# Performance work log

Measured on AMD Instinct MI355X. Metric: run time of the kernel, lower is better.

Reference implementation:

```python
import jax, jax.numpy as jnp
import numpy as np

B, N, C = 4, 1024, 1024
H, TD, MULT = 16, 256, 4
HD = C // H
MAX_LEN = 1024
EPS = 1e-5


def _layer_norm(x, g, b):
    m = jnp.mean(x, axis=-1, keepdims=True)
    v = jnp.mean((x - m) ** 2, axis=-1, keepdims=True)
    return (x - m) / jnp.sqrt(v + EPS) * g + b


def _skew(x):
    # x: [B,H,N,M] -> pad left on last dim, reshape, drop first row -> [B,H,N,M]
    b, h, n, m = x.shape
    x = jnp.pad(x, ((0, 0), (0, 0), (0, 0), (1, 0)))
    x = x.reshape(b, h, m + 1, n)
    return x[:, :, 1:, :]


def setup_inputs() -> dict:
    key = jax.random.key(0)
    ks = jax.random.split(key, 16)
    s = 0.02
    return {
        "x": jax.random.normal(ks[0], (B, N, C), jnp.float32),
        "t": jax.random.normal(ks[1], (B, TD), jnp.float32),
        "ln1_g": jnp.ones((C,), jnp.float32),
        "ln1_b": jnp.zeros((C,), jnp.float32),
        "qkv_w": jax.random.normal(ks[2], (C, 3 * C), jnp.float32) * s,
        "qkv_b": jnp.zeros((3 * C,), jnp.float32),
        "time_w": jax.random.normal(ks[3], (TD, 3 * C), jnp.float32) * s,
        "time_b": jnp.zeros((3 * C,), jnp.float32),
        "out_w": jax.random.normal(ks[4], (C, C), jnp.float32) * s,
        "out_b": jnp.zeros((C,), jnp.float32),
        "Er": jax.random.normal(ks[5], (MAX_LEN, HD), jnp.float32) * s,
        "ln2_g": jnp.ones((C,), jnp.float32),
        "ln2_b": jnp.zeros((C,), jnp.float32),
        "ff1_w": jax.random.normal(ks[6], (C, MULT * C), jnp.float32) * s,
        "ff1_b": jnp.zeros((MULT * C,), jnp.float32),
        "ff2_w": jax.random.normal(ks[7], (MULT * C, C), jnp.float32) * s,
        "ff2_b": jnp.zeros((C,), jnp.float32),
    }


def reference(x, t, ln1_g, ln1_b, qkv_w, qkv_b, time_w, time_b, out_w, out_b,
              Er, ln2_g, ln2_b, ff1_w, ff1_b, ff2_w, ff2_b):
    # ---- attention branch ----
    xn = _layer_norm(x, ln1_g, ln1_b)
    qkv = (xn @ qkv_w + qkv_b).reshape(B, N, 3, H, HD).transpose(2, 0, 3, 1, 4)
    q, k, v = qkv[0], qkv[1], qkv[2]  # [B,H,N,HD]
    tqkv = (t @ time_w + time_b).reshape(B, 1, 3, H, HD).transpose(2, 0, 3, 1, 4)
    q = q + tqkv[0]
    k = k + tqkv[1]
    v = v + tqkv[2]
    Er_n = Er[MAX_LEN - N:]  # [N,HD]
    rel = jnp.einsum('bhnd,md->bhnm', q, Er_n)
    rel = _skew(rel)
    scale = HD ** -0.5
    attn = jnp.einsum('bhnd,bhmd->bhnm', q, k) * scale + rel
    attn = jax.nn.softmax(attn, axis=-1)
    out = jnp.einsum('bhnm,bhmd->bhnd', attn, v)
    out = out.transpose(0, 2, 1, 3).reshape(B, N, C)
    x = x + (out @ out_w + out_b)
    # ---- FFN branch ----
    h = _layer_norm(x, ln2_g, ln2_b)
    h = jax.nn.gelu(h @ ff1_w + ff1_b, approximate=False)
    x = x + (h @ ff2_w + ff2_b)
    return x
```

## Files before the change

### kernel.cpp

```cpp
#include <hip/hip_runtime.h>
#include <hip/hip_bf16.h>

typedef __attribute__((ext_vector_type(8))) short short8;
typedef __attribute__((ext_vector_type(4))) float f32x4;
typedef __attribute__((ext_vector_type(16))) float f32x16;

#define DEV __device__ __forceinline__

DEV float bf2f(ushort u){ union { float f; unsigned int i; } x; x.i = ((unsigned int)u)<<16; return x.f; }
DEV ushort f2bf(float f){ union { float fl; unsigned int i; } x; x.fl = f; unsigned int r = x.i + 0x7fffu + ((x.i>>16)&1u); return (ushort)(r>>16); }

DEV void gl2lds16(const ushort* g, ushort* l){
  __builtin_amdgcn_global_load_lds((const __attribute__((address_space(1))) void*)g,
                                   (__attribute__((address_space(3))) void*)l, 16, 0, 0);
}
DEV f32x16 mfma32(short8 a, short8 b, f32x16 c){
  return __builtin_amdgcn_mfma_f32_32x32x16_bf16(a, b, c, 0, 0, 0);
}
DEV uint cvtpk(float lo, float hi){
  uint r; asm("v_cvt_pk_bf16_f32 %0, %1, %2" : "=v"(r) : "v"(lo), "v"(hi));
  return r;
}

__global__ void cvt_f2b(const float* __restrict__ in, ushort* __restrict__ out, int n){
  int i = blockIdx.x*blockDim.x + threadIdx.x;
  int stride = gridDim.x*blockDim.x;
  for (; i < n; i += stride) out[i] = f2bf(in[i]);
}

__global__ __launch_bounds__(256) void wt_cvt(const float* __restrict__ in, ushort* __restrict__ out,
                                              int K, int N, int ldk){
  const int n0 = blockIdx.x*64, k0 = blockIdx.y*64;
  __shared__ float T[64][65];
  const int tid = threadIdx.x;
  const int r = tid>>4, c = (tid&15)*4;
  #pragma unroll
  for (int p=0;p<4;p++){
    float4 v = *(const float4*)&in[(size_t)(k0 + p*16 + r)*N + n0 + c];
    T[p*16+r][c+0]=v.x; T[p*16+r][c+1]=v.y; T[p*16+r][c+2]=v.z; T[p*16+r][c+3]=v.w;
  }
  __syncthreads();
  #pragma unroll
  for (int p=0;p<4;p++){
    int n = p*16 + r;
    ushort u0 = f2bf(T[c+0][n]), u1 = f2bf(T[c+1][n]), u2 = f2bf(T[c+2][n]), u3 = f2bf(T[c+3][n]);
    ushort4 u = make_ushort4(u0,u1,u2,u3);
    *(ushort4*)&out[(size_t)(n0+n)*ldk + k0 + c] = u;
  }
}

__global__ __launch_bounds__(256) void vt_k(const ushort* __restrict__ qkv, ushort* __restrict__ vt){
  const int bh = blockIdx.y; const int b = bh>>4, h = bh&15;
  const int n0 = blockIdx.x*64;
  __shared__ ushort T[64][66];
  const int tid = threadIdx.x;
  const int r = tid>>3, c8 = (tid&7)*8;
  #pragma unroll
  for (int p=0;p<2;p++){
    int row = p*32 + r;
    short8 v = *(const short8*)&qkv[(size_t)(b*1024 + n0 + row)*3200 + 2048 + h*64 + c8];
    #pragma unroll
    for (int i=0;i<8;i++) T[row][c8+i] = ((ushort*)&v)[i];
  }
  __syncthreads();
  #pragma unroll
  for (int p=0;p<2;p++){
    int d = p*32 + r;
    union { ushort u[8]; short8 v; } o;
    #pragma unroll
    for (int i=0;i<8;i++) o.u[i] = T[c8+i][d];
    *(short8*)&vt[(size_t)(bh*64 + d)*1152 + n0 + c8] = o.v;
  }
}

__global__ __launch_bounds__(256) void ln_rows(const float* __restrict__ in,
                                               const float* __restrict__ g,
                                               const float* __restrict__ bta,
                                               ushort* __restrict__ out, int ldo){
  int row = blockIdx.x; int tid = threadIdx.x;
  const float* x = in + (size_t)row*1024;
  float v[4]; float s = 0.f;
  #pragma unroll
  for (int i=0;i<4;i++){ v[i] = x[tid + 256*i]; s += v[i]; }
  __shared__ float rbuf[256];
  rbuf[tid] = s; __syncthreads();
  for (int off=128; off>0; off>>=1){ if (tid<off) rbuf[tid]+=rbuf[tid+off]; __syncthreads(); }
  float mean = rbuf[0] * (1.f/1024.f);
  __syncthreads();
  float s2 = 0.f;
  #pragma unroll
  for (int i=0;i<4;i++){ float d=v[i]-mean; s2 += d*d; }
  rbuf[tid] = s2; __syncthreads();
  for (int off=128; off>0; off>>=1){ if (tid<off) rbuf[tid]+=rbuf[tid+off]; __syncthreads(); }
  float var = rbuf[0] * (1.f/1024.f);
  float rstd = rsqrtf(var + 1e-5f);
  #pragma unroll
  for (int i=0;i<4;i++){ int c = tid+256*i; out[(size_t)row*ldo+c] = f2bf((v[i]-mean)*rstd*g[c]+bta[c]); }
}

__global__ __launch_bounds__(256) void tq_gemm2(const float* __restrict__ t, const float* __restrict__ tw,
                                                const float* __restrict__ tb, float* __restrict__ tq){
  const int tid = threadIdx.x;
  const int j = blockIdx.x*64 + (tid & 63);
  const int sl = tid >> 6;
  float acc[4] = {0.f,0.f,0.f,0.f};
  for (int k = sl*64; k < sl*64+64; ++k){
    float wv = tw[(size_t)k*3072 + j];
    #pragma unroll
    for (int b=0;b<4;b++) acc[b] = fmaf(t[b*256+k], wv, acc[b]);
  }
  __shared__ float red[4][4][64];
  #pragma unroll
  for (int b=0;b<4;b++) red[sl][b][tid&63] = acc[b];
  __syncthreads();
  if (sl == 0){
    #pragma unroll
    for (int b=0;b<4;b++)
      tq[b*3072 + j] = red[0][b][tid&63] + red[1][b][tid&63] + red[2][b][tid&63] + red[3][b][tid&63] + tb[j];
  }
}

template<int EPI, int TN>
__global__ __launch_bounds__(256) void gemm4(
    const ushort* __restrict__ A, const ushort* __restrict__ Bt,
    const float* __restrict__ bias, const float* __restrict__ extra,
    ushort* __restrict__ outb, float* __restrict__ outf,
    int K, int lda, int ldb, int ldo, int lde, int nbx)
{
  constexpr int NJ = TN/32;
  __shared__ __align__(16) ushort Al[2][128*32];
  __shared__ __align__(16) ushort Bl[2][TN*32];
  const int nwg = gridDim.x, cpx = nwg >> 3;
  const int bid = blockIdx.x;
  const int swz = (bid & 7)*cpx + (bid >> 3);
  const int m0 = (swz / nbx)*128, n0 = (swz % nbx)*TN;
  const int tid = threadIdx.x, lane = tid & 63, wid = tid >> 6;
  const int wm = (wid&1)*64, wn = (wid>>1)*(TN/2);
  const int l15 = lane&15, l4 = lane>>4;
  f32x4 acc[4][NJ];
  #pragma unroll
  for (int i=0;i<4;i++)
    #pragma unroll
    for (int jx=0;jx<NJ;jx++){ acc[i][jx][0]=0.f; acc[i][jx][1]=0.f; acc[i][jx][2]=0.f; acc[i][jx][3]=0.f; }
  const ushort* a0p = A + (size_t)(m0 + (tid>>2))*lda + (tid&3)*8;
  const ushort* a1p = A + (size_t)(m0 + 64 + (tid>>2))*lda + (tid&3)*8;
  const ushort* b0p = Bt + (size_t)(n0 + (tid>>2))*ldb + (tid&3)*8;
  const ushort* b1p = nullptr;
  if constexpr (TN==128) b1p = Bt + (size_t)(n0 + 64 + (tid>>2))*ldb + (tid&3)*8;
  const int lsl = tid*8, lsh = (tid+256)*8;

  gl2lds16(a0p, &Al[0][lsl]);
  gl2lds16(a1p, &Al[0][lsh]);
  gl2lds16(b0p, &Bl[0][lsl]);
  if constexpr (TN==128) gl2lds16(b1p, &Bl[0][lsh]);
  __syncthreads();

  const int nk = K >> 5;
  for (int it=0; it<nk; ++it){
    const int cur = it & 1;
    ushort* Ac = Al[cur];  ushort* Bc = Bl[cur];
    if (it+1 < nk){
      const int k1 = (it+1) << 5;
      gl2lds16(a0p + k1, &Al[cur^1][lsl]);
      gl2lds16(a1p + k1, &Al[cur^1][lsh]);
      gl2lds16(b0p + k1, &Bl[cur^1][lsl]);
      if constexpr (TN==128) gl2lds16(b1p + k1, &Bl[cur^1][lsh]);
    }
    short8 af[4], bfr[NJ];
    #pragma unroll
    for (int mi=0;mi<4;mi++) af[mi]  = *(const short8*)&Ac[(wm + mi*16 + l15)*32 + l4*8];
    #pragma unroll
    for (int nj=0;nj<NJ;nj++) bfr[nj] = *(const short8*)&Bc[(wn + nj*16 + l15)*32 + l4*8];
    #pragma unroll
    for (int mi=0;mi<4;mi++)
      #pragma unroll
      for (int nj=0;nj<NJ;nj++)
        acc[mi][nj] = __builtin_amdgcn_mfma_f32_16x16x32_bf16(af[mi], bfr[nj], acc[mi][nj], 0,0,0);
    __syncthreads();
  }
  #pragma unroll
  for (int mi=0;mi<4;mi++)
    #pragma unroll
    for (int nj=0;nj<NJ;nj++)
      #pragma unroll
      for (int j=0;j<4;j++){
        int row = m0 + wm + mi*16 + l4*4 + j;
        int col = n0 + wn + nj*16 + l15;
        float v = acc[mi][nj][j] + bias[col];
        if constexpr (EPI==0){ v += extra[(size_t)(row>>10)*lde + col]; outb[(size_t)row*ldo+col] = f2bf(v); }
        else if constexpr (EPI==1){ v += extra[(size_t)row*lde + col]; outf[(size_t)row*ldo+col] = v; }
        else { v = 0.5f*v*(1.f+erff(v*0.70710678118f)); outb[(size_t)row*ldo+col] = f2bf(v); }
      }
}


__global__ __launch_bounds__(256) void relskew(
    const ushort* __restrict__ qkv, const ushort* __restrict__ Er,
    ushort* __restrict__ srel)
{
  const int bid0 = blockIdx.x;
  const int bid = ((bid0 & 7) << 9) | (bid0 >> 3);
  const int rt = bid & 63, h = (bid>>6)&15, b = bid>>10;
  const int bh = b*16 + h;
  const int r0 = rt*16;
  const int tid = threadIdx.x, w = tid>>6, lane = tid&63;
  const int l15 = lane&15, l4 = lane>>4;
  __shared__ __align__(16) ushort T[17*1032];
  ushort* srb = srel + (size_t)bh*1024*1040;

  if (tid < 17){
    int tgt = r0 - 1 + tid;
    int c = tgt + 1;
    if (tgt >= 0 && c <= 1023) T[tid*1032 + c] = 0;
  }
  const ushort* Qp = qkv + (size_t)b*1024*3200 + h*64;
  short8 qa0 = *(const short8*)(Qp + (size_t)(r0+l15)*3200 + l4*8);
  short8 qa1 = *(const short8*)(Qp + (size_t)(r0+l15)*3200 + 32 + l4*8);
  for (int t=0;t<16;++t){
    const int et = w*16 + t;
    short8 e0 = *(const short8*)(Er + (size_t)(et*16+l15)*64 + l4*8);
    short8 e1 = *(const short8*)(Er + (size_t)(et*16+l15)*64 + 32 + l4*8);
    f32x4 a0 = {0.f,0.f,0.f,0.f};
    a0 = __builtin_amdgcn_mfma_f32_16x16x32_bf16(qa0, e0, a0, 0,0,0);
    a0 = __builtin_amdgcn_mfma_f32_16x16x32_bf16(qa1, e1, a0, 0,0,0);
    const int e = et*16 + l15;
    #pragma unroll
    for (int j=0;j<4;j++){
      int lr = 4*l4 + j;
      int r = r0 + lr;
      ushort v = f2bf(a0[j] * 1.4426950408f);
      bool below = (e >= 1023 - r);
      int ldsrow = below ? (lr + 1) : lr;
      int c = below ? (e + r - 1023) : (e + r + 1);
      T[ldsrow*1032 + c] = v;
    }
  }
  __syncthreads();
  const int c4 = tid*4;
  for (int i=0;i<17;++i){
    int tgt = r0 - 1 + i;
    if (tgt < 0) continue;
    int lo = (i==0) ? (r0+1) : 0;
    int hh = (i==16) ? min(r0+16,1023) : 1023;
    if (c4 >= lo && c4+3 <= hh){
      uint2 vv = *(const uint2*)&T[i*1032 + c4];
      *(uint2*)(srb + (size_t)tgt*1040 + c4) = vv;
    } else if (c4 <= hh && c4+3 >= lo){
      #pragma unroll
      for (int k2=0;k2<4;k2++){
        int c = c4 + k2;
        if (c >= lo && c <= hh) srb[(size_t)tgt*1040 + c] = T[i*1032 + c];
      }
    }
  }
}

__global__ __launch_bounds__(256) void attn6(
    const ushort* __restrict__ qkv, const ushort* __restrict__ srel,
    const ushort* __restrict__ Vt, ushort* __restrict__ out)
{
  const int bid0 = blockIdx.x;
  const int swz = (bid0 & 7)*64 + (bid0 >> 3);
  const int bh = swz >> 3, b = bh >> 4, h = bh & 15;
  const int rblk = (swz & 7)*128;
  const int tid = threadIdx.x, w = tid >> 6, lane = tid & 63;
  const int l31 = lane & 31, hi = lane >> 5;
  const int r = rblk + w*32 + l31;
  const ushort* Qp = qkv + (size_t)b*1024*3200 + h*64;
  const ushort* Kp = Qp + 1024;
  const ushort* Vp = Vt + (size_t)bh*64*1152;
  const ushort* Bp = srel + (size_t)bh*1024*1040 + (size_t)r*1040 + hi*4;

  short8 qf0 = *(const short8*)(Qp + (size_t)r*3200 +      hi*8);
  short8 qf1 = *(const short8*)(Qp + (size_t)r*3200 + 16 + hi*8);
  short8 qf2 = *(const short8*)(Qp + (size_t)r*3200 + 32 + hi*8);
  short8 qf3 = *(const short8*)(Qp + (size_t)r*3200 + 48 + hi*8);

  f32x16 O0 = {}, O1 = {};
  float m = -3e38f, lsum = 0.f;

  short8 kA0 = *(const short8*)(Kp + (size_t)l31*3200 +      hi*8);
  short8 kA1 = *(const short8*)(Kp + (size_t)l31*3200 + 16 + hi*8);
  short8 kA2 = *(const short8*)(Kp + (size_t)l31*3200 + 32 + hi*8);
  short8 kA3 = *(const short8*)(Kp + (size_t)l31*3200 + 48 + hi*8);
  short8 kB0, kB1, kB2, kB3;

  auto step = [&](short8& ka0, short8& ka1, short8& ka2, short8& ka3,
                  short8& kn0, short8& kn1, short8& kn2, short8& kn3, int t){
    const int c0 = t*32;
    if (t < 31){
      const ushort* kp = Kp + (size_t)(c0 + 32 + l31)*3200 + hi*8;
      kn0 = *(const short8*)(kp);
      kn1 = *(const short8*)(kp + 16);
      kn2 = *(const short8*)(kp + 32);
      kn3 = *(const short8*)(kp + 48);
    }
    ushort4 bs[4];
    #pragma unroll
    for (int rq=0;rq<4;rq++) bs[rq] = *(const ushort4*)(Bp + c0 + rq*8);
    short8 v00 = *(const short8*)(Vp + (size_t)l31*1152      + c0 +      hi*8);
    short8 v01 = *(const short8*)(Vp + (size_t)l31*1152      + c0 + 16 + hi*8);
    short8 v10 = *(const short8*)(Vp + (size_t)(32+l31)*1152 + c0 +      hi*8);
    short8 v11 = *(const short8*)(Vp + (size_t)(32+l31)*1152 + c0 + 16 + hi*8);
    f32x16 S = {};
    S = mfma32(ka0, qf0, S);
    S = mfma32(ka1, qf1, S);
    S = mfma32(ka2, qf2, S);
    S = mfma32(ka3, qf3, S);
    float p[16];
    float tmax = -3e38f;
    #pragma unroll
    for (int rq=0;rq<4;rq++)
      #pragma unroll
      for (int j=0;j<4;j++){
        float v = fmaf(S[rq*4+j], 0.18033688f, bf2f(((const ushort*)&bs[rq])[j]));
        p[rq*4+j] = v;
        tmax = fmaxf(tmax, v);
      }
    tmax = fmaxf(tmax, __shfl_xor(tmax, 32, 64));
    if (!__all(tmax <= m + 8.f)){
      float mn = fmaxf(m, tmax);
      float scl = __builtin_amdgcn_exp2f(m - mn);
      m = mn; lsum *= scl;
      #pragma unroll
      for (int i=0;i<16;i++){ O0[i]*=scl; O1[i]*=scl; }
    }
    float tsum = 0.f;
    #pragma unroll
    for (int reg=0;reg<16;reg++){ p[reg] = __builtin_amdgcn_exp2f(p[reg]-m); tsum += p[reg]; }
    lsum += tsum;
    uint W00=cvtpk(p[0],p[1]),   W01=cvtpk(p[2],p[3]);
    uint W10=cvtpk(p[4],p[5]),   W11=cvtpk(p[6],p[7]);
    uint W20=cvtpk(p[8],p[9]),   W21=cvtpk(p[10],p[11]);
    uint W30=cvtpk(p[12],p[13]), W31=cvtpk(p[14],p[15]);
    uint x00 = (uint)__shfl_xor((int)(hi? W00 : W10), 32, 64);
    uint x01 = (uint)__shfl_xor((int)(hi? W01 : W11), 32, 64);
    uint x10 = (uint)__shfl_xor((int)(hi? W20 : W30), 32, 64);
    uint x11 = (uint)__shfl_xor((int)(hi? W21 : W31), 32, 64);
    union { uint u[4]; short8 v; } pf0, pf1;
    pf0.u[0] = hi ? x00 : W00;  pf0.u[1] = hi ? x01 : W01;
    pf0.u[2] = hi ? W10 : x00;  pf0.u[3] = hi ? W11 : x01;
    pf1.u[0] = hi ? x10 : W20;  pf1.u[1] = hi ? x11 : W21;
    pf1.u[2] = hi ? W30 : x10;  pf1.u[3] = hi ? W31 : x11;
    O0 = mfma32(v00, pf0.v, O0);
    O0 = mfma32(v01, pf1.v, O0);
    O1 = mfma32(v10, pf0.v, O1);
    O1 = mfma32(v11, pf1.v, O1);
  };
  for (int t=0;t<32;t+=2){
    step(kA0,kA1,kA2,kA3, kB0,kB1,kB2,kB3, t);
    step(kB0,kB1,kB2,kB3, kA0,kA1,kA2,kA3, t+1);
  }
  float inv = 1.f/(lsum + __shfl_xor(lsum, 32, 64));
  ushort* op = out + ((size_t)(b*1024 + r))*1152 + h*64;
  #pragma unroll
  for (int rq=0;rq<4;rq++)
    #pragma unroll
    for (int s=0;s<2;s++){
      int reg = rq*4 + s*2;
      uint w0 = cvtpk(O0[reg]*inv, O0[reg+1]*inv);
      uint w1 = cvtpk(O1[reg]*inv, O1[reg+1]*inv);
      int d = rq*8 + hi*4 + s*2;
      *(uint*)(op + d) = w0;
      *(uint*)(op + 32 + d) = w1;
    }
}

__global__ __launch_bounds__(256,3) void attn5(
    const ushort* __restrict__ qkv, const ushort* __restrict__ Er,
    const ushort* __restrict__ Vt, ushort* __restrict__ out)
{
  const int bid0 = blockIdx.x;
  const int bid = ((bid0 & 7) << 9) | (bid0 >> 3);
  const int rt = bid & 63, h = (bid>>6)&15, b = bid>>10;
  const int bh = b*16 + h;
  const int r0 = rt*16;
  const int tid = threadIdx.x, w = tid>>6, lane = tid&63;
  const int l15 = lane&15, l4 = lane>>4;

  __shared__ ushort RRF[17568];
  __shared__ __align__(16) ushort shp[4][16][88];
  __shared__ float mlbuf[4][2][16];

  const size_t base = (size_t)b*1024*3200 + (size_t)h*64;
  const ushort* Qp = qkv + base;
  const ushort* Kp = qkv + base + 1024;
  const ushort* Vp = Vt + (size_t)bh*64*1152;

  if (tid < 16) RRF[(tid+1)*1033] = 0;

  short8 qa[2], qb[2];
  const int q1 = min(r0 + 16 + l15, 1023);
  #pragma unroll
  for (int ks=0; ks<2; ++ks){
    qa[ks] = *(const short8*)(Qp + (size_t)(r0 + l15)*3200 + ks*32 + l4*8);
    qb[ks] = *(const short8*)(Qp + (size_t)q1*3200 + ks*32 + l4*8);
  }
  short8 e0 = *(const short8*)(Er + (size_t)(w*256 + l15)*64 + l4*8);
  short8 e1 = *(const short8*)(Er + (size_t)(w*256 + l15)*64 + 32 + l4*8);
  for (int t=0; t<16; ++t){
    const int et = w*16 + t;
    short8 c0v = e0, c1v = e1;
    if (t < 15){
      e0 = *(const short8*)(Er + (size_t)((et+1)*16 + l15)*64 + l4*8);
      e1 = *(const short8*)(Er + (size_t)((et+1)*16 + l15)*64 + 32 + l4*8);
    }
    f32x4 a0 = {0.f,0.f,0.f,0.f}, a1 = {0.f,0.f,0.f,0.f};
    a0 = __builtin_amdgcn_mfma_f32_16x16x32_bf16(qa[0], c0v, a0, 0,0,0);
    a1 = __builtin_amdgcn_mfma_f32_16x16x32_bf16(qb[0], c0v, a1, 0,0,0);
    a0 = __builtin_amdgcn_mfma_f32_16x16x32_bf16(qa[1], c1v, a0, 0,0,0);
    a1 = __builtin_amdgcn_mfma_f32_16x16x32_bf16(qb[1], c1v, a1, 0,0,0);
    const int e = et*16 + l15;
    #pragma unroll
    for (int j=0;j<4;j++) RRF[(l4*4+j)*1033 + 1 + e] = f2bf(a0[j]);
    if (l4 == 0) RRF[16*1033 + 1 + e] = f2bf(a1[0]);
  }
  __syncthreads();

  float m = -1e30f, lsum = 0.f;
  f32x4 Oacc[4];
  #pragma unroll
  for (int n2=0;n2<4;n2++){ Oacc[n2][0]=0.f; Oacc[n2][1]=0.f; Oacc[n2][2]=0.f; Oacc[n2][3]=0.f; }
  const int dl = 4*l4 - l15;
  const int rbase = l15*1033;
  const int c0base = w*256;

  short8 ka[2][4][2];
  #pragma unroll
  for (int f=0;f<4;f++)
    #pragma unroll
    for (int ks=0;ks<2;ks++)
      ka[0][f][ks] = *(const short8*)(Kp + (size_t)(c0base + f*16 + l15)*3200 + ks*32 + l4*8);

  #pragma unroll
  for (int t=0;t<4;++t){
    const int cur = t&1;
    const int c0 = c0base + t*64;
    float skf[16];
    #pragma unroll
    for (int f=0;f<4;f++)
      #pragma unroll
      for (int j=0;j<4;j++){
        int d = (c0 + f*16 + j - r0) + dl;
        int off = (d<=0) ? (1024+d) : (1032+d);
        skf[f*4+j] = bf2f(RRF[rbase + off]);
      }
    f32x4 S[4];
    #pragma unroll
    for (int f=0;f<4;f++){
      S[f][0]=0.f; S[f][1]=0.f; S[f][2]=0.f; S[f][3]=0.f;
      #pragma unroll
      for (int ks=0;ks<2;ks++)
        S[f] = __builtin_amdgcn_mfma_f32_16x16x32_bf16(ka[cur][f][ks], qa[ks], S[f], 0,0,0);
    }
    if (t < 3){
      const int c2 = c0 + 64;
      #pragma unroll
      for (int f=0;f<4;f++)
        #pragma unroll
        for (int ks=0;ks<2;ks++)
          ka[cur^1][f][ks] = *(const short8*)(Kp + (size_t)(c2 + f*16 + l15)*3200 + ks*32 + l4*8);
    }
    short8 va[2][4];
    #pragma unroll
    for (int ks=0;ks<2;ks++)
      #pragma unroll
      for (int n2=0;n2<4;n2++)
        va[ks][n2] = *(const short8*)(Vp + (size_t)(n2*16 + l15)*1152 + c0 + ks*32 + l4*8);
    float tm[4];
    #pragma unroll
    for (int f=0;f<4;f++){
      float v0 = fmaf(S[f][0], 0.125f, skf[f*4+0]);
      float v1 = fmaf(S[f][1], 0.125f, skf[f*4+1]);
      float v2 = fmaf(S[f][2], 0.125f, skf[f*4+2]);
      float v3 = fmaf(S[f][3], 0.125f, skf[f*4+3]);
      S[f][0]=v0; S[f][1]=v1; S[f][2]=v2; S[f][3]=v3;
      tm[f] = fmaxf(fmaxf(v0,v1), fmaxf(v2,v3));
    }
    float tmax = fmaxf(fmaxf(tm[0],tm[1]), fmaxf(tm[2],tm[3]));
    tmax = fmaxf(tmax, __shfl_xor(tmax, 16, 64));
    tmax = fmaxf(tmax, __shfl_xor(tmax, 32, 64));
    const float mn = fmaxf(m, tmax);
    const float scl = __expf(m - mn);
    m = mn;
    float tsum = 0.f;
    #pragma unroll
    for (int f=0;f<4;f++){
      float p0 = __expf(S[f][0]-m), p1 = __expf(S[f][1]-m), p2 = __expf(S[f][2]-m), p3 = __expf(S[f][3]-m);
      tsum += (p0+p1)+(p2+p3);
      ushort4 pw = make_ushort4(f2bf(p0), f2bf(p1), f2bf(p2), f2bf(p3));
      *(ushort4*)&shp[w][l15][f*16 + l4*4] = pw;
    }
    tsum += __shfl_xor(tsum, 16, 64);
    tsum += __shfl_xor(tsum, 32, 64);
    lsum = lsum*scl + tsum;
    #pragma unroll
    for (int n2=0;n2<4;n2++)
      #pragma unroll
      for (int j=0;j<4;j++) Oacc[n2][j] *= scl;
    #pragma unroll
    for (int ks=0; ks<2; ++ks){
      short8 pb = *(const short8*)&shp[w][l15][ks*32 + l4*8];
      #pragma unroll
      for (int n2=0; n2<4; ++n2)
        Oacc[n2] = __builtin_amdgcn_mfma_f32_16x16x32_bf16(va[ks][n2], pb, Oacc[n2], 0,0,0);
    }
  }
  #pragma unroll
  for (int n2=0;n2<4;n2++){
    ushort4 ow = make_ushort4(f2bf(Oacc[n2][0]), f2bf(Oacc[n2][1]), f2bf(Oacc[n2][2]), f2bf(Oacc[n2][3]));
    *(ushort4*)&shp[w][l15][n2*16 + l4*4] = ow;
  }
  if (l4 == 0){ mlbuf[w][0][l15] = m; mlbuf[w][1][l15] = lsum; }
  __syncthreads();
  {
    const int row = tid>>4, hb = (tid&15)*4;
    float M2 = mlbuf[0][0][row];
    #pragma unroll
    for (int w2=1;w2<4;w2++) M2 = fmaxf(M2, mlbuf[w2][0][row]);
    float den = 0.f, num[4] = {0.f,0.f,0.f,0.f};
    #pragma unroll
    for (int w2=0;w2<4;w2++){
      float e = __expf(mlbuf[w2][0][row] - M2);
      den += mlbuf[w2][1][row]*e;
      ushort4 ov = *(const ushort4*)&shp[w2][row][hb];
      num[0] += bf2f(ov.x)*e; num[1] += bf2f(ov.y)*e; num[2] += bf2f(ov.z)*e; num[3] += bf2f(ov.w)*e;
    }
    float invd = 1.f/den;
    ushort4 u;
    u.x = f2bf(num[0]*invd); u.y = f2bf(num[1]*invd); u.z = f2bf(num[2]*invd); u.w = f2bf(num[3]*invd);
    *(ushort4*)&out[((size_t)(b*1024 + r0 + row))*1152 + h*64 + hb] = u;
  }
}

extern "C" void kernel_launch(void* const* d_in, const int* in_sizes, int n_in,
                              void* d_out, int out_size, void* d_ws, size_t ws_size,
                              hipStream_t stream)
{
  const float* x    = (const float*)d_in[0];
  const float* t    = (const float*)d_in[1];
  const float* ln1g = (const float*)d_in[2];
  const float* ln1b = (const float*)d_in[3];
  const float* qkvw = (const float*)d_in[4];
  const float* qkvb = (const float*)d_in[5];
  const float* timew= (const float*)d_in[6];
  const float* timeb= (const float*)d_in[7];
  const float* outw = (const float*)d_in[8];
  const float* outbv= (const float*)d_in[9];
  const float* Er   = (const float*)d_in[10];
  const float* ln2g = (const float*)d_in[11];
  const float* ln2b = (const float*)d_in[12];
  const float* ff1w = (const float*)d_in[13];
  const float* ff1b = (const float*)d_in[14];
  const float* ff2w = (const float*)d_in[15];
  const float* ff2b = (const float*)d_in[16];
  float* o = (float*)d_out;

  char* ws = (char*)d_ws;
  ushort* qkvw_t = (ushort*)(ws);
  ushort* outw_t = (ushort*)(ws + 7077888);
  ushort* ff1w_t = (ushort*)(ws + 9437184);
  ushort* ff2w_t = (ushort*)(ws + 18874368);
  ushort* er_b   = (ushort*)(ws + 27525120);
  float*  tq     = (float*) (ws + 27656192);
  ushort* bufA   = (ushort*)(ws + 27705344);
  ushort* vt     = (ushort*)(ws + 37142528);
  ushort* bufB   = (ushort*)(ws + 46579712);
  ushort* srel   = (ushort*)(ws + 81182720);
  const bool big = ws_size >= 217497600ull;

  wt_cvt<<<dim3(48,16),256,0,stream>>>(qkvw, qkvw_t, 1024, 3072, 1152);
  wt_cvt<<<dim3(16,16),256,0,stream>>>(outw, outw_t, 1024, 1024, 1152);
  wt_cvt<<<dim3(64,16),256,0,stream>>>(ff1w, ff1w_t, 1024, 4096, 1152);
  wt_cvt<<<dim3(16,64),256,0,stream>>>(ff2w, ff2w_t, 4096, 1024, 4224);
  cvt_f2b<<<256,256,0,stream>>>(Er, er_b, 65536);

  ln_rows<<<4096,256,0,stream>>>(x, ln1g, ln1b, bufA, 1152);
  tq_gemm2<<<48,256,0,stream>>>(t, timew, timeb, tq);
  gemm4<0,128><<<768,256,0,stream>>>(bufA, qkvw_t, qkvb, tq, bufB, nullptr,
                                     1024, 1152, 1152, 3200, 3072, 24);
  vt_k<<<dim3(16,64),256,0,stream>>>(bufB, vt);
  if (big){
    relskew<<<4096,256,0,stream>>>(bufB, er_b, srel);
    attn6<<<512,256,0,stream>>>(bufB, srel, vt, bufA);
  } else {
    attn5<<<4096,256,0,stream>>>(bufB, er_b, vt, bufA);
  }
  gemm4<1,64><<<512,256,0,stream>>>(bufA, outw_t, outbv, x, nullptr, o,
                                    1024, 1152, 1152, 1024, 1024, 16);
  ln_rows<<<4096,256,0,stream>>>(o, ln2g, ln2b, bufA, 1152);
  gemm4<2,128><<<1024,256,0,stream>>>(bufA, ff1w_t, ff1b, nullptr, bufB, nullptr,
                                      1024, 1152, 1152, 4224, 0, 32);
  gemm4<1,64><<<512,256,0,stream>>>(bufB, ff2w_t, ff2b, o, nullptr, o,
                                    4096, 4224, 4224, 1024, 1024, 16);
}
```

Measured before the change: 412.3 us.

## Fuse relative-position skew into attention kernel with split-KV over waves

Replaces the separate relskew kernel, which wrote a full skewed relative-position bias tensor to global memory, and the attn6 consumer with a single attn7 kernel. attn7 computes Q·Er for a 32-row tile into LDS and reads the skewed bias directly from LDS with an index remap. Each of the four waves handles a quarter of the keys, and the partial results are merged through LDS with a max/sum combine. This removes a large global write/read round trip and one launch. In exchange it adds LDS pressure, which limits occupancy, plus per-element LDS gathers and a cross-wave reduction.

```diff
diff --git a/kernel.cpp b/kernel.cpp
--- a/kernel.cpp
+++ b/kernel.cpp
@@ -193,111 +193,111 @@
       }
 }
 
-
-__global__ __launch_bounds__(256) void relskew(
+__global__ __launch_bounds__(256) void attn7(
     const ushort* __restrict__ qkv, const ushort* __restrict__ Er,
-    ushort* __restrict__ srel)
-{
-  const int bid0 = blockIdx.x;
-  const int bid = ((bid0 & 7) << 9) | (bid0 >> 3);
-  const int rt = bid & 63, h = (bid>>6)&15, b = bid>>10;
-  const int bh = b*16 + h;
-  const int r0 = rt*16;
-  const int tid = threadIdx.x, w = tid>>6, lane = tid&63;
-  const int l15 = lane&15, l4 = lane>>4;
-  __shared__ __align__(16) ushort T[17*1032];
-  ushort* srb = srel + (size_t)bh*1024*1040;
-
-  if (tid < 17){
-    int tgt = r0 - 1 + tid;
-    int c = tgt + 1;
-    if (tgt >= 0 && c <= 1023) T[tid*1032 + c] = 0;
-  }
-  const ushort* Qp = qkv + (size_t)b*1024*3200 + h*64;
-  short8 qa0 = *(const short8*)(Qp + (size_t)(r0+l15)*3200 + l4*8);
-  short8 qa1 = *(const short8*)(Qp + (size_t)(r0+l15)*3200 + 32 + l4*8);
-  for (int t=0;t<16;++t){
-    const int et = w*16 + t;
-    short8 e0 = *(const short8*)(Er + (size_t)(et*16+l15)*64 + l4*8);
-    short8 e1 = *(const short8*)(Er + (size_t)(et*16+l15)*64 + 32 + l4*8);
-    f32x4 a0 = {0.f,0.f,0.f,0.f};
-    a0 = __builtin_amdgcn_mfma_f32_16x16x32_bf16(qa0, e0, a0, 0,0,0);
-    a0 = __builtin_amdgcn_mfma_f32_16x16x32_bf16(qa1, e1, a0, 0,0,0);
-    const int e = et*16 + l15;
-    #pragma unroll
-    for (int j=0;j<4;j++){
-      int lr = 4*l4 + j;
-      int r = r0 + lr;
-      ushort v = f2bf(a0[j] * 1.4426950408f);
-      bool below = (e >= 1023 - r);
-      int ldsrow = below ? (lr + 1) : lr;
-      int c = below ? (e + r - 1023) : (e + r + 1);
-      T[ldsrow*1032 + c] = v;
-    }
-  }
-  __syncthreads();
-  const int c4 = tid*4;
-  for (int i=0;i<17;++i){
-    int tgt = r0 - 1 + i;
-    if (tgt < 0) continue;
-    int lo = (i==0) ? (r0+1) : 0;
-    int hh = (i==16) ? min(r0+16,1023) : 1023;
-    if (c4 >= lo && c4+3 <= hh){
-      uint2 vv = *(const uint2*)&T[i*1032 + c4];
-      *(uint2*)(srb + (size_t)tgt*1040 + c4) = vv;
-    } else if (c4 <= hh && c4+3 >= lo){
-      #pragma unroll
-      for (int k2=0;k2<4;k2++){
-        int c = c4 + k2;
-        if (c >= lo && c <= hh) srb[(size_t)tgt*1040 + c] = T[i*1032 + c];
-      }
-    }
-  }
-}
-
-__global__ __launch_bounds__(256) void attn6(
-    const ushort* __restrict__ qkv, const ushort* __restrict__ srel,
     const ushort* __restrict__ Vt, ushort* __restrict__ out)
 {
   const int bid0 = blockIdx.x;
-  const int swz = (bid0 & 7)*64 + (bid0 >> 3);
-  const int bh = swz >> 3, b = bh >> 4, h = bh & 15;
-  const int rblk = (swz & 7)*128;
+  const int swz = (bid0 & 7)*256 + (bid0 >> 3);
+  const int bh = swz >> 5, b = bh >> 4, h = bh & 15;
+  const int rt = swz & 31;
+  const int r0 = rt*32;
   const int tid = threadIdx.x, w = tid >> 6, lane = tid & 63;
   const int l31 = lane & 31, hi = lane >> 5;
-  const int r = rblk + w*32 + l31;
+
+  __shared__ __align__(16) ushort RRF[34176];
+  ushort* Obuf = RRF;
+  float*  ml   = (float*)(RRF + 8704);
+
   const ushort* Qp = qkv + (size_t)b*1024*3200 + h*64;
   const ushort* Kp = Qp + 1024;
   const ushort* Vp = Vt + (size_t)bh*64*1152;
-  const ushort* Bp = srel + (size_t)bh*1024*1040 + (size_t)r*1040 + hi*4;
-
+
+  const int r = r0 + l31;
   short8 qf0 = *(const short8*)(Qp + (size_t)r*3200 +      hi*8);
   short8 qf1 = *(const short8*)(Qp + (size_t)r*3200 + 16 + hi*8);
   short8 qf2 = *(const short8*)(Qp + (size_t)r*3200 + 32 + hi*8);
   short8 qf3 = *(const short8*)(Qp + (size_t)r*3200 + 48 + hi*8);
 
+  if (tid < 32) RRF[tid*1036 + 1035] = 0;
+
+  for (int t=0; t<8; ++t){
+    const int e0 = w*256 + t*32;
+    const ushort* ep = Er + (size_t)(e0 + l31)*64 + hi*8;
+    short8 ea0 = *(const short8*)(ep);
+    short8 ea1 = *(const short8*)(ep + 16);
+    short8 ea2 = *(const short8*)(ep + 32);
+    short8 ea3 = *(const short8*)(ep + 48);
+    f32x16 acc = {};
+    acc = mfma32(ea0, qf0, acc);
+    acc = mfma32(ea1, qf1, acc);
+    acc = mfma32(ea2, qf2, acc);
+    acc = mfma32(ea3, qf3, acc);
+    #pragma unroll
+    for (int q=0;q<4;q++){
+      int e = e0 + 8*q + 4*hi;
+      uint2 wv;
+      wv.x = cvtpk(acc[4*q+0]*1.4426950408f, acc[4*q+1]*1.4426950408f);
+      wv.y = cvtpk(acc[4*q+2]*1.4426950408f, acc[4*q+3]*1.4426950408f);
+      *(uint2*)&RRF[l31*1036 + e] = wv;
+    }
+  }
+  {
+    const int q32r = min(r0 + 32, 1023);
+    const ushort* q32 = Qp + (size_t)q32r*3200;
+    const int e4 = tid*4;
+    float a[4] = {0.f,0.f,0.f,0.f};
+    #pragma unroll
+    for (int c8=0;c8<8;c8++){
+      short8 qv = *(const short8*)(q32 + c8*8);
+      float qx[8];
+      #pragma unroll
+      for (int i=0;i<8;i++) qx[i] = bf2f(((ushort*)&qv)[i]);
+      #pragma unroll
+      for (int e=0;e<4;e++){
+        short8 ev = *(const short8*)(Er + (size_t)(e4+e)*64 + c8*8);
+        #pragma unroll
+        for (int i=0;i<8;i++) a[e] = fmaf(qx[i], bf2f(((ushort*)&ev)[i]), a[e]);
+      }
+    }
+    uint2 wv;
+    wv.x = cvtpk(a[0]*1.4426950408f, a[1]*1.4426950408f);
+    wv.y = cvtpk(a[2]*1.4426950408f, a[3]*1.4426950408f);
+    *(uint2*)&RRF[32*1036 + e4] = wv;
+  }
+  __syncthreads();
+
+  const int rbase = l31*1036;
+  const int kvbase = w*256;
   f32x16 O0 = {}, O1 = {};
   float m = -3e38f, lsum = 0.f;
 
-  short8 kA0 = *(const short8*)(Kp + (size_t)l31*3200 +      hi*8);
-  short8 kA1 = *(const short8*)(Kp + (size_t)l31*3200 + 16 + hi*8);
-  short8 kA2 = *(const short8*)(Kp + (size_t)l31*3200 + 32 + hi*8);
-  short8 kA3 = *(const short8*)(Kp + (size_t)l31*3200 + 48 + hi*8);
+  short8 kA0 = *(const short8*)(Kp + (size_t)(kvbase + l31)*3200 +      hi*8);
+  short8 kA1 = *(const short8*)(Kp + (size_t)(kvbase + l31)*3200 + 16 + hi*8);
+  short8 kA2 = *(const short8*)(Kp + (size_t)(kvbase + l31)*3200 + 32 + hi*8);
+  short8 kA3 = *(const short8*)(Kp + (size_t)(kvbase + l31)*3200 + 48 + hi*8);
   short8 kB0, kB1, kB2, kB3;
 
   auto step = [&](short8& ka0, short8& ka1, short8& ka2, short8& ka3,
                   short8& kn0, short8& kn1, short8& kn2, short8& kn3, int t){
-    const int c0 = t*32;
-    if (t < 31){
+    const int c0 = kvbase + t*32;
+    if (t < 7){
       const ushort* kp = Kp + (size_t)(c0 + 32 + l31)*3200 + hi*8;
       kn0 = *(const short8*)(kp);
       kn1 = *(const short8*)(kp + 16);
       kn2 = *(const short8*)(kp + 32);
       kn3 = *(const short8*)(kp + 48);
     }
-    ushort4 bs[4];
-    #pragma unroll
-    for (int rq=0;rq<4;rq++) bs[rq] = *(const ushort4*)(Bp + c0 + rq*8);
+    ushort bs[16];
+    #pragma unroll
+    for (int q=0;q<4;q++)
+      #pragma unroll
+      for (int j=0;j<4;j++){
+        int c = c0 + 8*q + 4*hi + j;
+        int d = c - r;
+        int off = (d<=0) ? (1023+d) : (1034+d);
+        bs[4*q+j] = RRF[rbase + off];
+      }
     short8 v00 = *(const short8*)(Vp + (size_t)l31*1152      + c0 +      hi*8);
     short8 v01 = *(const short8*)(Vp + (size_t)l31*1152      + c0 + 16 + hi*8);
     short8 v10 = *(const short8*)(Vp + (size_t)(32+l31)*1152 + c0 +      hi*8);
@@ -310,13 +310,11 @@
     float p[16];
     float tmax = -3e38f;
     #pragma unroll
-    for (int rq=0;rq<4;rq++)
-      #pragma unroll
-      for (int j=0;j<4;j++){
-        float v = fmaf(S[rq*4+j], 0.18033688f, bf2f(((const ushort*)&bs[rq])[j]));
-        p[rq*4+j] = v;
-        tmax = fmaxf(tmax, v);
-      }
+    for (int i=0;i<16;i++){
+      float v = fmaf(S[i], 0.18033688f, bf2f(bs[i]));
+      p[i] = v;
+      tmax = fmaxf(tmax, v);
+    }
     tmax = fmaxf(tmax, __shfl_xor(tmax, 32, 64));
     if (!__all(tmax <= m + 8.f)){
       float mn = fmaxf(m, tmax);
@@ -327,7 +325,7 @@
     }
     float tsum = 0.f;
     #pragma unroll
-    for (int reg=0;reg<16;reg++){ p[reg] = __builtin_amdgcn_exp2f(p[reg]-m); tsum += p[reg]; }
+    for (int i=0;i<16;i++){ p[i] = __builtin_amdgcn_exp2f(p[i]-m); tsum += p[i]; }
     lsum += tsum;
     uint W00=cvtpk(p[0],p[1]),   W01=cvtpk(p[2],p[3]);
     uint W10=cvtpk(p[4],p[5]),   W11=cvtpk(p[6],p[7]);
@@ -347,189 +345,48 @@
     O1 = mfma32(v10, pf0.v, O1);
     O1 = mfma32(v11, pf1.v, O1);
   };
-  for (int t=0;t<32;t+=2){
+  for (int t=0;t<8;t+=2){
     step(kA0,kA1,kA2,kA3, kB0,kB1,kB2,kB3, t);
     step(kB0,kB1,kB2,kB3, kA0,kA1,kA2,kA3, t+1);
   }
-  float inv = 1.f/(lsum + __shfl_xor(lsum, 32, 64));
-  ushort* op = out + ((size_t)(b*1024 + r))*1152 + h*64;
-  #pragma unroll
-  for (int rq=0;rq<4;rq++)
-    #pragma unroll
-    for (int s=0;s<2;s++){
-      int reg = rq*4 + s*2;
-      uint w0 = cvtpk(O0[reg]*inv, O0[reg+1]*inv);
-      uint w1 = cvtpk(O1[reg]*inv, O1[reg+1]*inv);
-      int d = rq*8 + hi*4 + s*2;
-      *(uint*)(op + d) = w0;
-      *(uint*)(op + 32 + d) = w1;
-    }
-}
-
-__global__ __launch_bounds__(256,3) void attn5(
-    const ushort* __restrict__ qkv, const ushort* __restrict__ Er,
-    const ushort* __restrict__ Vt, ushort* __restrict__ out)
-{
-  const int bid0 = blockIdx.x;
-  const int bid = ((bid0 & 7) << 9) | (bid0 >> 3);
-  const int rt = bid & 63, h = (bid>>6)&15, b = bid>>10;
-  const int bh = b*16 + h;
-  const int r0 = rt*16;
-  const int tid = threadIdx.x, w = tid>>6, lane = tid&63;
-  const int l15 = lane&15, l4 = lane>>4;
-
-  __shared__ ushort RRF[17568];
-  __shared__ __align__(16) ushort shp[4][16][88];
-  __shared__ float mlbuf[4][2][16];
-
-  const size_t base = (size_t)b*1024*3200 + (size_t)h*64;
-  const ushort* Qp = qkv + base;
-  const ushort* Kp = qkv + base + 1024;
-  const ushort* Vp = Vt + (size_t)bh*64*1152;
-
-  if (tid < 16) RRF[(tid+1)*1033] = 0;
-
-  short8 qa[2], qb[2];
-  const int q1 = min(r0 + 16 + l15, 1023);
-  #pragma unroll
-  for (int ks=0; ks<2; ++ks){
-    qa[ks] = *(const short8*)(Qp + (size_t)(r0 + l15)*3200 + ks*32 + l4*8);
-    qb[ks] = *(const short8*)(Qp + (size_t)q1*3200 + ks*32 + l4*8);
-  }
-  short8 e0 = *(const short8*)(Er + (size_t)(w*256 + l15)*64 + l4*8);
-  short8 e1 = *(const short8*)(Er + (size_t)(w*256 + l15)*64 + 32 + l4*8);
-  for (int t=0; t<16; ++t){
-    const int et = w*16 + t;
-    short8 c0v = e0, c1v = e1;
-    if (t < 15){
-      e0 = *(const short8*)(Er + (size_t)((et+1)*16 + l15)*64 + l4*8);
-      e1 = *(const short8*)(Er + (size_t)((et+1)*16 + l15)*64 + 32 + l4*8);
-    }
-    f32x4 a0 = {0.f,0.f,0.f,0.f}, a1 = {0.f,0.f,0.f,0.f};
-    a0 = __builtin_amdgcn_mfma_f32_16x16x32_bf16(qa[0], c0v, a0, 0,0,0);
-    a1 = __builtin_amdgcn_mfma_f32_16x16x32_bf16(qb[0], c0v, a1, 0,0,0);
-    a0 = __builtin_amdgcn_mfma_f32_16x16x32_bf16(qa[1], c1v, a0, 0,0,0);
-    a1 = __builtin_amdgcn_mfma_f32_16x16x32_bf16(qb[1], c1v, a1, 0,0,0);
-    const int e = et*16 + l15;
-    #pragma unroll
-    for (int j=0;j<4;j++) RRF[(l4*4+j)*1033 + 1 + e] = f2bf(a0[j]);
-    if (l4 == 0) RRF[16*1033 + 1 + e] = f2bf(a1[0]);
-  }
-  __syncthreads();
-
-  float m = -1e30f, lsum = 0.f;
-  f32x4 Oacc[4];
-  #pragma unroll
-  for (int n2=0;n2<4;n2++){ Oacc[n2][0]=0.f; Oacc[n2][1]=0.f; Oacc[n2][2]=0.f; Oacc[n2][3]=0.f; }
-  const int dl = 4*l4 - l15;
-  const int rbase = l15*1033;
-  const int c0base = w*256;
-
-  short8 ka[2][4][2];
-  #pragma unroll
-  for (int f=0;f<4;f++)
-    #pragma unroll
-    for (int ks=0;ks<2;ks++)
-      ka[0][f][ks] = *(const short8*)(Kp + (size_t)(c0base + f*16 + l15)*3200 + ks*32 + l4*8);
-
-  #pragma unroll
-  for (int t=0;t<4;++t){
-    const int cur = t&1;
-    const int c0 = c0base + t*64;
-    float skf[16];
-    #pragma unroll
-    for (int f=0;f<4;f++)
-      #pragma unroll
-      for (int j=0;j<4;j++){
-        int d = (c0 + f*16 + j - r0) + dl;
-        int off = (d<=0) ? (1024+d) : (1032+d);
-        skf[f*4+j] = bf2f(RRF[rbase + off]);
-      }
-    f32x4 S[4];
-    #pragma unroll
-    for (int f=0;f<4;f++){
-      S[f][0]=0.f; S[f][1]=0.f; S[f][2]=0.f; S[f][3]=0.f;
-      #pragma unroll
-      for (int ks=0;ks<2;ks++)
-        S[f] = __builtin_amdgcn_mfma_f32_16x16x32_bf16(ka[cur][f][ks], qa[ks], S[f], 0,0,0);
-    }
-    if (t < 3){
-      const int c2 = c0 + 64;
-      #pragma unroll
-      for (int f=0;f<4;f++)
-        #pragma unroll
-        for (int ks=0;ks<2;ks++)
-          ka[cur^1][f][ks] = *(const short8*)(Kp + (size_t)(c2 + f*16 + l15)*3200 + ks*32 + l4*8);
-    }
-    short8 va[2][4];
-    #pragma unroll
-    for (int ks=0;ks<2;ks++)
-      #pragma unroll
-      for (int n2=0;n2<4;n2++)
-        va[ks][n2] = *(const short8*)(Vp + (size_t)(n2*16 + l15)*1152 + c0 + ks*32 + l4*8);
-    float tm[4];
-    #pragma unroll
-    for (int f=0;f<4;f++){
-      float v0 = fmaf(S[f][0], 0.125f, skf[f*4+0]);
-      float v1 = fmaf(S[f][1], 0.125f, skf[f*4+1]);
-      float v2 = fmaf(S[f][2], 0.125f, skf[f*4+2]);
-      float v3 = fmaf(S[f][3], 0.125f, skf[f*4+3]);
-      S[f][0]=v0; S[f][1]=v1; S[f][2]=v2; S[f][3]=v3;
-      tm[f] = fmaxf(fmaxf(v0,v1), fmaxf(v2,v3));
-    }
-    float tmax = fmaxf(fmaxf(tm[0],tm[1]), fmaxf(tm[2],tm[3]));
-    tmax = fmaxf(tmax, __shfl_xor(tmax, 16, 64));
-    tmax = fmaxf(tmax, __shfl_xor(tmax, 32, 64));
-    const float mn = fmaxf(m, tmax);
-    const float scl = __expf(m - mn);
-    m = mn;
-    float tsum = 0.f;
-    #pragma unroll
-    for (int f=0;f<4;f++){
-      float p0 = __expf(S[f][0]-m), p1 = __expf(S[f][1]-m), p2 = __expf(S[f][2]-m), p3 = __expf(S[f][3]-m);
-      tsum += (p0+p1)+(p2+p3);
-      ushort4 pw = make_ushort4(f2bf(p0), f2bf(p1), f2bf(p2), f2bf(p3));
-      *(ushort4*)&shp[w][l15][f*16 + l4*4] = pw;
-    }
-    tsum += __shfl_xor(tsum, 16, 64);
-    tsum += __shfl_xor(tsum, 32, 64);
-    lsum = lsum*scl + tsum;
-    #pragma unroll
-    for (int n2=0;n2<4;n2++)
-      #pragma unroll
-      for (int j=0;j<4;j++) Oacc[n2][j] *= scl;
-    #pragma unroll
-    for (int ks=0; ks<2; ++ks){
-      short8 pb = *(const short8*)&shp[w][l15][ks*32 + l4*8];
-      #pragma unroll
-      for (int n2=0; n2<4; ++n2)
-        Oacc[n2] = __builtin_amdgcn_mfma_f32_16x16x32_bf16(va[ks][n2], pb, Oacc[n2], 0,0,0);
-    }
-  }
-  #pragma unroll
-  for (int n2=0;n2<4;n2++){
-    ushort4 ow = make_ushort4(f2bf(Oacc[n2][0]), f2bf(Oacc[n2][1]), f2bf(Oacc[n2][2]), f2bf(Oacc[n2][3]));
-    *(ushort4*)&shp[w][l15][n2*16 + l4*4] = ow;
-  }
-  if (l4 == 0){ mlbuf[w][0][l15] = m; mlbuf[w][1][l15] = lsum; }
+  lsum = lsum + __shfl_xor(lsum, 32, 64);
+
+  __syncthreads();
+  #pragma unroll
+  for (int q=0;q<4;q++){
+    int d = 8*q + 4*hi;
+    uint2 w0, w1;
+    w0.x = cvtpk(O0[4*q+0], O0[4*q+1]); w0.y = cvtpk(O0[4*q+2], O0[4*q+3]);
+    w1.x = cvtpk(O1[4*q+0], O1[4*q+1]); w1.y = cvtpk(O1[4*q+2], O1[4*q+3]);
+    *(uint2*)&Obuf[(w*32 + l31)*68 + d] = w0;
+    *(uint2*)&Obuf[(w*32 + l31)*68 + 32 + d] = w1;
+  }
+  if (hi == 0){ ml[(w*2+0)*32 + l31] = m; ml[(w*2+1)*32 + l31] = lsum; }
   __syncthreads();
   {
-    const int row = tid>>4, hb = (tid&15)*4;
-    float M2 = mlbuf[0][0][row];
-    #pragma unroll
-    for (int w2=1;w2<4;w2++) M2 = fmaxf(M2, mlbuf[w2][0][row]);
-    float den = 0.f, num[4] = {0.f,0.f,0.f,0.f};
+    const int row = tid >> 3, ds8 = (tid & 7)*8;
+    float M = ml[0*64 + row];
+    #pragma unroll
+    for (int w2=1;w2<4;w2++) M = fmaxf(M, ml[w2*64 + row]);
+    float den = 0.f, num[8] = {0.f,0.f,0.f,0.f,0.f,0.f,0.f,0.f};
     #pragma unroll
     for (int w2=0;w2<4;w2++){
-      float e = __expf(mlbuf[w2][0][row] - M2);
-      den += mlbuf[w2][1][row]*e;
-      ushort4 ov = *(const ushort4*)&shp[w2][row][hb];
-      num[0] += bf2f(ov.x)*e; num[1] += bf2f(ov.y)*e; num[2] += bf2f(ov.z)*e; num[3] += bf2f(ov.w)*e;
-    }
-    float invd = 1.f/den;
-    ushort4 u;
-    u.x = f2bf(num[0]*invd); u.y = f2bf(num[1]*invd); u.z = f2bf(num[2]*invd); u.w = f2bf(num[3]*invd);
-    *(ushort4*)&out[((size_t)(b*1024 + r0 + row))*1152 + h*64 + hb] = u;
+      float e2 = __builtin_amdgcn_exp2f(ml[w2*64 + row] - M);
+      den += ml[w2*64 + 32 + row]*e2;
+      uint2 o0 = *(const uint2*)&Obuf[(w2*32 + row)*68 + ds8];
+      uint2 o1 = *(const uint2*)&Obuf[(w2*32 + row)*68 + ds8 + 4];
+      const ushort* ou0 = (const ushort*)&o0;
+      const ushort* ou1 = (const ushort*)&o1;
+      #pragma unroll
+      for (int i=0;i<4;i++){ num[i] += bf2f(ou0[i])*e2; num[4+i] += bf2f(ou1[i])*e2; }
+    }
+    float inv = 1.f/den;
+    union { uint u[4]; short8 v; } ov;
+    ov.u[0] = cvtpk(num[0]*inv, num[1]*inv);
+    ov.u[1] = cvtpk(num[2]*inv, num[3]*inv);
+    ov.u[2] = cvtpk(num[4]*inv, num[5]*inv);
+    ov.u[3] = cvtpk(num[6]*inv, num[7]*inv);
+    *(short8*)&out[((size_t)(b*1024 + r0 + row))*1152 + h*64 + ds8] = ov.v;
   }
 }
 
@@ -566,8 +423,6 @@
   ushort* bufA   = (ushort*)(ws + 27705344);
   ushort* vt     = (ushort*)(ws + 37142528);
   ushort* bufB   = (ushort*)(ws + 46579712);
-  ushort* srel   = (ushort*)(ws + 81182720);
-  const bool big = ws_size >= 217497600ull;
 
   wt_cvt<<<dim3(48,16),256,0,stream>>>(qkvw, qkvw_t, 1024, 3072, 1152);
   wt_cvt<<<dim3(16,16),256,0,stream>>>(outw, outw_t, 1024, 1024, 1152);
@@ -580,12 +435,7 @@
   gemm4<0,128><<<768,256,0,stream>>>(bufA, qkvw_t, qkvb, tq, bufB, nullptr,
                                      1024, 1152, 1152, 3200, 3072, 24);
   vt_k<<<dim3(16,64),256,0,stream>>>(bufB, vt);
-  if (big){
-    relskew<<<4096,256,0,stream>>>(bufB, er_b, srel);
-    attn6<<<512,256,0,stream>>>(bufB, srel, vt, bufA);
-  } else {
-    attn5<<<4096,256,0,stream>>>(bufB, er_b, vt, bufA);
-  }
+  attn7<<<2048,256,0,stream>>>(bufB, er_b, vt, bufA);
   gemm4<1,64><<<512,256,0,stream>>>(bufA, outw_t, outbv, x, nullptr, o,
                                     1024, 1152, 1152, 1024, 1024, 16);
   ln_rows<<<4096,256,0,stream>>>(o, ln2g, ln2b, bufA, 1152);
```

Result: faster. 395.1 us (-4.2%).
